# Kernel optimization log

Hardware: AMD Instinct MI355X
Metric: run time of the kernel (lower is better)

The kernel has to match this reference:

```python
import jax, jax.numpy as jnp
import numpy as np

B, C, S, L = 8, 512, 2048, 8921


def setup_inputs() -> dict:
    key = jax.random.key(0)
    k1, k2, k3, k4, k5 = jax.random.split(key, 5)
    return {
        "encoded": jax.random.normal(k1, (B, C, S), dtype=jnp.float32),
        "W_attn": jax.random.normal(k2, (L, C), dtype=jnp.float32) * 0.02,
        "b_attn": jax.random.normal(k3, (L,), dtype=jnp.float32) * 0.02,
        "W_cls": jax.random.normal(k4, (L, C), dtype=jnp.float32) * 0.02,
        "b_cls": jax.random.normal(k5, (L,), dtype=jnp.float32) * 0.02,
    }


def reference(encoded, W_attn, b_attn, W_cls, b_cls):
    # encoded: (B, C, S). Linear over channels after transpose -> scores (B, S, L)
    scores = jnp.einsum("bcs,lc->bsl", encoded, W_attn) + b_attn
    # softmax over the sequence dimension (dim=1 of (B, S, L))
    weights = jax.nn.softmax(scores, axis=1)
    # context: (B, L, S) @ (B, S, C) -> (B, L, C)
    context = jnp.einsum("bsl,bcs->blc", weights, encoded)
    # per-label diagonal classifier: elementwise multiply with (L, C) weight, reduce C
    logits = jnp.sum(context * W_cls, axis=2) + b_cls  # (B, L)
    return logits
```

## Files before the change

kernel.cpp:

```cpp
#include <hip/hip_runtime.h>
#include <hip/hip_bf16.h>
#include <stdint.h>

#define B_ 8
#define C_ 512
#define S_ 2048
#define L_ 8921
#define LTILE 128
#define NLT 70
#define BS 128
#define SCHUNK 512
#define NSC 4
#define STILES 4
#define BK 32
#define CITERS 16

using f32x4 = __attribute__((ext_vector_type(4))) float;
using s16x8 = __attribute__((ext_vector_type(8))) short;

static __device__ __forceinline__ unsigned short f2bf(float f) {
    union { float f; uint32_t u; } a; a.f = f;
    uint32_t u = a.u;
    return (unsigned short)((u + 0x7fffu + ((u >> 16) & 1u)) >> 16);
}

__global__ void cvt_w(const float* __restrict__ src, unsigned short* __restrict__ dst, int n4) {
    int i = blockIdx.x * 256 + threadIdx.x;
    if (i >= n4) return;
    float4 v = ((const float4*)src)[i];
    ushort4 o;
    o.x = f2bf(v.x); o.y = f2bf(v.y); o.z = f2bf(v.z); o.w = f2bf(v.w);
    ((ushort4*)dst)[i] = o;
}

__global__ void cvt_e(const float* __restrict__ enc, unsigned short* __restrict__ ebt) {
    __shared__ float tile[64][65];
    int x = blockIdx.x;
    int ct = (x & 7) * 64;
    int st = ((x >> 3) & 31) * 64;
    int b  = x >> 8;
    int t = threadIdx.x;
    const float* src = enc + (size_t)b * C_ * S_;
    #pragma unroll
    for (int it = 0; it < 16; ++it) {
        int idx = it * 256 + t;
        int rc = idx >> 6, rs = idx & 63;
        tile[rc][rs] = src[(size_t)(ct + rc) * S_ + st + rs];
    }
    __syncthreads();
    unsigned short* dst = ebt + (size_t)b * S_ * C_;
    #pragma unroll
    for (int it = 0; it < 16; ++it) {
        int idx = it * 256 + t;
        int rs = idx >> 6, rc = idx & 63;
        dst[(size_t)(st + rs) * C_ + ct + rc] = f2bf(tile[rc][rs]);
    }
}

__global__ __launch_bounds__(256, 2) void attn_main(
    const unsigned short* __restrict__ ebt,
    const unsigned short* __restrict__ wa,
    const unsigned short* __restrict__ wc,
    float* __restrict__ pnum, float* __restrict__ pden)
{
    __shared__ __align__(16) unsigned char smem[24576];
    unsigned char* sWa = smem;
    unsigned char* sWc = smem + 8192;
    unsigned char* sEt = smem + 16384;

    const int tid  = threadIdx.x;
    const int lane = tid & 63;
    const int wave = tid >> 6;

    const int x  = blockIdx.x;
    const int sc = x & 3;
    const int lt = (x >> 2) % NLT;
    const int b  = x / (NSC * NLT);

    const int l0 = lt * LTILE;
    const int wm = wave >> 1, wn = wave & 1;
    const int mbase = wm * 64, nbase = wn * 64;

    const int rowInSlab = lane >> 2;
    const int chunkGlb  = (lane & 3) ^ ((lane >> 3) & 3);
    const int fragKs  = (((lane >> 4) ^ ((lane >> 1) & 3)) << 4);
    const int fragRow = (lane & 15) << 6;

    float numAcc[4][4];
    float denAcc[4][4];
    #pragma unroll
    for (int i = 0; i < 4; ++i)
        #pragma unroll
        for (int r = 0; r < 4; ++r) { numAcc[i][r] = 0.f; denAcc[i][r] = 0.f; }

    for (int st = 0; st < STILES; ++st) {
        const int s0 = sc * SCHUNK + st * BS;
        f32x4 accS[4][4], accV[4][4];
        #pragma unroll
        for (int i = 0; i < 4; ++i)
            #pragma unroll
            for (int j = 0; j < 4; ++j) {
                accS[i][j] = (f32x4){0.f, 0.f, 0.f, 0.f};
                accV[i][j] = (f32x4){0.f, 0.f, 0.f, 0.f};
            }

        for (int ci = 0; ci < CITERS; ++ci) {
            const int c0 = ci * BK;
            __syncthreads();
            #pragma unroll
            for (int j = 0; j < 6; ++j) {
                const int slab = wave * 6 + j;
                const unsigned short* gsrc;
                unsigned char* ldst;
                if (slab < 8) {
                    int gl = l0 + slab * 16 + rowInSlab; if (gl > L_ - 1) gl = L_ - 1;
                    gsrc = wa + (size_t)gl * C_ + c0 + chunkGlb * 8;
                    ldst = sWa + slab * 1024;
                } else if (slab < 16) {
                    int g = slab - 8;
                    int gl = l0 + g * 16 + rowInSlab; if (gl > L_ - 1) gl = L_ - 1;
                    gsrc = wc + (size_t)gl * C_ + c0 + chunkGlb * 8;
                    ldst = sWc + g * 1024;
                } else {
                    int g = slab - 16;
                    int gs = s0 + g * 16 + rowInSlab;
                    gsrc = ebt + ((size_t)b * S_ + gs) * C_ + c0 + chunkGlb * 8;
                    ldst = sEt + g * 1024;
                }
                __builtin_amdgcn_global_load_lds(
                    (__attribute__((address_space(1))) void*)gsrc,
                    (__attribute__((address_space(3))) void*)ldst,
                    16, 0, 0);
            }
            __syncthreads();

            s16x8 fa[4], fc[4], fe[4];
            #pragma unroll
            for (int mf = 0; mf < 4; ++mf) {
                const int off = ((mbase + mf * 16) << 6) + fragRow + fragKs;
                fa[mf] = *(const s16x8*)(sWa + off);
                fc[mf] = *(const s16x8*)(sWc + off);
            }
            #pragma unroll
            for (int nf = 0; nf < 4; ++nf) {
                const int off = ((nbase + nf * 16) << 6) + fragRow + fragKs;
                fe[nf] = *(const s16x8*)(sEt + off);
            }
            #pragma unroll
            for (int mf = 0; mf < 4; ++mf)
                #pragma unroll
                for (int nf = 0; nf < 4; ++nf) {
                    accS[mf][nf] = __builtin_amdgcn_mfma_f32_16x16x32_bf16(fa[mf], fe[nf], accS[mf][nf], 0, 0, 0);
                    accV[mf][nf] = __builtin_amdgcn_mfma_f32_16x16x32_bf16(fc[mf], fe[nf], accV[mf][nf], 0, 0, 0);
                }
        }

        #pragma unroll
        for (int mf = 0; mf < 4; ++mf)
            #pragma unroll
            for (int nf = 0; nf < 4; ++nf)
                #pragma unroll
                for (int r = 0; r < 4; ++r) {
                    float e = __expf(accS[mf][nf][r]);
                    denAcc[mf][r] += e;
                    numAcc[mf][r] += e * accV[mf][nf][r];
                }
    }

    __syncthreads();
    float* pn = (float*)smem;
    float* pd = (float*)(smem + 1024);
    #pragma unroll
    for (int mf = 0; mf < 4; ++mf)
        #pragma unroll
        for (int r = 0; r < 4; ++r) {
            float n = numAcc[mf][r], d = denAcc[mf][r];
            n += __shfl_xor(n, 1);  d += __shfl_xor(d, 1);
            n += __shfl_xor(n, 2);  d += __shfl_xor(d, 2);
            n += __shfl_xor(n, 4);  d += __shfl_xor(d, 4);
            n += __shfl_xor(n, 8);  d += __shfl_xor(d, 8);
            if ((lane & 15) == 0) {
                int lrow = mf * 16 + (lane >> 4) * 4 + r;
                pn[wave * 64 + lrow] = n;
                pd[wave * 64 + lrow] = d;
            }
        }
    __syncthreads();
    if (tid < LTILE) {
        int half = tid >> 6;
        int lrow = tid & 63;
        float n = pn[(half * 2) * 64 + lrow] + pn[(half * 2 + 1) * 64 + lrow];
        float d = pd[(half * 2) * 64 + lrow] + pd[(half * 2 + 1) * 64 + lrow];
        size_t idx = ((size_t)((b * NLT + lt) * NSC + sc)) * LTILE + tid;
        pnum[idx] = n; pden[idx] = d;
    }
}

__global__ void finalize(const float* __restrict__ pnum, const float* __restrict__ pden,
                         const float* __restrict__ bcls, float* __restrict__ out) {
    int gid = blockIdx.x * 256 + threadIdx.x;
    if (gid >= B_ * L_) return;
    int b = gid / L_, l = gid - b * L_;
    int lt = l >> 7, row = l & 127;
    float n = 0.f, d = 0.f;
    #pragma unroll
    for (int s = 0; s < NSC; ++s) {
        size_t idx = ((size_t)((b * NLT + lt) * NSC + s)) * LTILE + row;
        n += pnum[idx];
        d += pden[idx];
    }
    out[gid] = n / d + bcls[l];
}

extern "C" void kernel_launch(void* const* d_in, const int* in_sizes, int n_in,
                              void* d_out, int out_size, void* d_ws, size_t ws_size,
                              hipStream_t stream) {
    (void)in_sizes; (void)n_in; (void)out_size; (void)ws_size;
    const float* enc  = (const float*)d_in[0];
    const float* Wa   = (const float*)d_in[1];
    const float* Wc   = (const float*)d_in[3];
    const float* bcls = (const float*)d_in[4];

    unsigned char* ws = (unsigned char*)d_ws;
    const size_t oEbt = 0;
    const size_t oWa  = oEbt + 16777216;
    const size_t oWc  = oWa + 9136128;
    const size_t oPn  = oWc + 9136128;
    const size_t oPd  = oPn + 1146880;

    unsigned short* ebt  = (unsigned short*)(ws + oEbt);
    unsigned short* waBf = (unsigned short*)(ws + oWa);
    unsigned short* wcBf = (unsigned short*)(ws + oWc);
    float* pnum = (float*)(ws + oPn);
    float* pden = (float*)(ws + oPd);

    const int n4 = (L_ * C_) / 4;
    cvt_w<<<(n4 + 255) / 256, 256, 0, stream>>>(Wa, waBf, n4);
    cvt_w<<<(n4 + 255) / 256, 256, 0, stream>>>(Wc, wcBf, n4);
    cvt_e<<<B_ * 32 * 8, 256, 0, stream>>>(enc, ebt);
    attn_main<<<B_ * NLT * NSC, 256, 0, stream>>>(ebt, waBf, wcBf, pnum, pden);
    finalize<<<(B_ * L_ + 255) / 256, 256, 0, stream>>>(pnum, pden, bcls, (float*)d_out);
}
```

Before: 478.3 us.

## Restructure attention GEMM: register-resident weight fragments, double-buffered LDS encoded tiles

Each wave now owns 32 label rows across the full 128-column s-tile. It loads its W_attn and W_cls fragments straight from global memory into registers and prefetches them one step ahead, so only the encoded tile is staged in LDS. That tile is double-buffered with a deeper K step of 64, which halves barriers and removes LDS traffic for the weights. Block order is remapped so that blocks sharing a label tile run together, for L2 reuse of the weights. In exchange the kernel carries more accumulator registers (16 accumulator tiles per wave) and relies on global loads to cover latency.

```diff
diff --git a/kernel.cpp b/kernel.cpp
--- a/kernel.cpp
+++ b/kernel.cpp
@@ -11,9 +11,8 @@
 #define BS 128
 #define SCHUNK 512
 #define NSC 4
-#define STILES 4
-#define BK 32
-#define CITERS 16
+#define BK 64
+#define ROUNDS 32
 
 using f32x4 = __attribute__((ext_vector_type(4))) float;
 using s16x8 = __attribute__((ext_vector_type(8))) short;
@@ -63,115 +62,135 @@
     const unsigned short* __restrict__ wc,
     float* __restrict__ pnum, float* __restrict__ pden)
 {
-    __shared__ __align__(16) unsigned char smem[24576];
-    unsigned char* sWa = smem;
-    unsigned char* sWc = smem + 8192;
-    unsigned char* sEt = smem + 16384;
+    __shared__ __align__(16) unsigned char sE[32768];
 
     const int tid  = threadIdx.x;
     const int lane = tid & 63;
     const int wave = tid >> 6;
 
     const int x  = blockIdx.x;
-    const int sc = x & 3;
-    const int lt = (x >> 2) % NLT;
-    const int b  = x / (NSC * NLT);
-
+    const int lt = x >> 5;
+    const int rb = x & 31;
+    const int b  = rb >> 2;
+    const int sc = rb & 3;
     const int l0 = lt * LTILE;
-    const int wm = wave >> 1, wn = wave & 1;
-    const int mbase = wm * 64, nbase = wn * 64;
-
-    const int rowInSlab = lane >> 2;
-    const int chunkGlb  = (lane & 3) ^ ((lane >> 3) & 3);
-    const int fragKs  = (((lane >> 4) ^ ((lane >> 1) & 3)) << 4);
-    const int fragRow = (lane & 15) << 6;
-
-    float numAcc[4][4];
-    float denAcc[4][4];
-    #pragma unroll
-    for (int i = 0; i < 4; ++i)
-        #pragma unroll
-        for (int r = 0; r < 4; ++r) { numAcc[i][r] = 0.f; denAcc[i][r] = 0.f; }
-
-    for (int st = 0; st < STILES; ++st) {
-        const int s0 = sc * SCHUNK + st * BS;
-        f32x4 accS[4][4], accV[4][4];
-        #pragma unroll
-        for (int i = 0; i < 4; ++i)
-            #pragma unroll
-            for (int j = 0; j < 4; ++j) {
-                accS[i][j] = (f32x4){0.f, 0.f, 0.f, 0.f};
-                accV[i][j] = (f32x4){0.f, 0.f, 0.f, 0.f};
-            }
-
-        for (int ci = 0; ci < CITERS; ++ci) {
-            const int c0 = ci * BK;
-            __syncthreads();
-            #pragma unroll
-            for (int j = 0; j < 6; ++j) {
-                const int slab = wave * 6 + j;
-                const unsigned short* gsrc;
-                unsigned char* ldst;
-                if (slab < 8) {
-                    int gl = l0 + slab * 16 + rowInSlab; if (gl > L_ - 1) gl = L_ - 1;
-                    gsrc = wa + (size_t)gl * C_ + c0 + chunkGlb * 8;
-                    ldst = sWa + slab * 1024;
-                } else if (slab < 16) {
-                    int g = slab - 8;
-                    int gl = l0 + g * 16 + rowInSlab; if (gl > L_ - 1) gl = L_ - 1;
-                    gsrc = wc + (size_t)gl * C_ + c0 + chunkGlb * 8;
-                    ldst = sWc + g * 1024;
-                } else {
-                    int g = slab - 16;
-                    int gs = s0 + g * 16 + rowInSlab;
-                    gsrc = ebt + ((size_t)b * S_ + gs) * C_ + c0 + chunkGlb * 8;
-                    ldst = sEt + g * 1024;
-                }
-                __builtin_amdgcn_global_load_lds(
-                    (__attribute__((address_space(1))) void*)gsrc,
-                    (__attribute__((address_space(3))) void*)ldst,
-                    16, 0, 0);
-            }
-            __syncthreads();
-
-            s16x8 fa[4], fc[4], fe[4];
-            #pragma unroll
-            for (int mf = 0; mf < 4; ++mf) {
-                const int off = ((mbase + mf * 16) << 6) + fragRow + fragKs;
-                fa[mf] = *(const s16x8*)(sWa + off);
-                fc[mf] = *(const s16x8*)(sWc + off);
-            }
-            #pragma unroll
-            for (int nf = 0; nf < 4; ++nf) {
-                const int off = ((nbase + nf * 16) << 6) + fragRow + fragKs;
-                fe[nf] = *(const s16x8*)(sEt + off);
-            }
-            #pragma unroll
-            for (int mf = 0; mf < 4; ++mf)
+
+    int rowOff[2];
+    #pragma unroll
+    for (int mf = 0; mf < 2; ++mf) {
+        int gl = l0 + wave * 32 + mf * 16 + (lane & 15);
+        if (gl > L_ - 1) gl = L_ - 1;
+        rowOff[mf] = gl * C_ + ((lane >> 4) << 3);
+    }
+
+    const size_t ebase = (size_t)b * S_ * C_;
+    const int kgsrcE = (((lane & 7) ^ ((lane >> 3) & 7)) << 3);
+    const int rowPart = (lane & 15) << 7;
+    const int laneQ = lane >> 4;
+    const int laneX = lane & 7;
+
+    struct W4 { s16x8 a0, a1, c0, c1; };
+    auto loadW = [&](int rr, int k) -> W4 {
+        const int co = ((rr & 7) << 6) + (k << 5);
+        W4 w;
+        w.a0 = *(const s16x8*)(wa + rowOff[0] + co);
+        w.a1 = *(const s16x8*)(wa + rowOff[1] + co);
+        w.c0 = *(const s16x8*)(wc + rowOff[0] + co);
+        w.c1 = *(const s16x8*)(wc + rowOff[1] + co);
+        return w;
+    };
+
+    auto stageE = [&](int rr2) {
+        const int c0s = (rr2 & 7) << 6;
+        const int sBase = sc * SCHUNK + (rr2 >> 3) * BS;
+        unsigned char* dbase = sE + ((rr2 & 1) << 14);
+        #pragma unroll
+        for (int jj = 0; jj < 4; ++jj) {
+            const int j = wave * 4 + jj;
+            const int sg = sBase + j * 8 + (lane >> 3);
+            const unsigned short* g = ebt + ebase + (size_t)sg * C_ + c0s + kgsrcE;
+            __builtin_amdgcn_global_load_lds(
+                (__attribute__((address_space(1))) void*)g,
+                (__attribute__((address_space(3))) void*)(dbase + j * 1024),
+                16, 0, 0);
+        }
+    };
+
+    f32x4 accS[2][8], accV[2][8];
+    #pragma unroll
+    for (int mf = 0; mf < 2; ++mf)
+        #pragma unroll
+        for (int nf = 0; nf < 8; ++nf) {
+            accS[mf][nf] = (f32x4){0.f, 0.f, 0.f, 0.f};
+            accV[mf][nf] = (f32x4){0.f, 0.f, 0.f, 0.f};
+        }
+    float numAcc[2][4], denAcc[2][4];
+    #pragma unroll
+    for (int mf = 0; mf < 2; ++mf)
+        #pragma unroll
+        for (int r = 0; r < 4; ++r) { numAcc[mf][r] = 0.f; denAcc[mf][r] = 0.f; }
+
+    stageE(0);
+    W4 wcur = loadW(0, 0);
+
+    for (int rr = 0; rr < ROUNDS; ++rr) {
+        __syncthreads();
+        if (rr + 1 < ROUNDS) stageE(rr + 1);
+        W4 wnxt = loadW(rr, 1);
+
+        const unsigned char* fb = sE + ((rr & 1) << 14);
+        {
+            s16x8 fe[8];
+            #pragma unroll
+            for (int nf = 0; nf < 8; ++nf) {
+                const int off = (nf << 11) + rowPart + ((((0 * 4) + laneQ) ^ laneX) << 4);
+                fe[nf] = *(const s16x8*)(fb + off);
+            }
+            #pragma unroll
+            for (int nf = 0; nf < 8; ++nf) {
+                accS[0][nf] = __builtin_amdgcn_mfma_f32_16x16x32_bf16(wcur.a0, fe[nf], accS[0][nf], 0, 0, 0);
+                accS[1][nf] = __builtin_amdgcn_mfma_f32_16x16x32_bf16(wcur.a1, fe[nf], accS[1][nf], 0, 0, 0);
+                accV[0][nf] = __builtin_amdgcn_mfma_f32_16x16x32_bf16(wcur.c0, fe[nf], accV[0][nf], 0, 0, 0);
+                accV[1][nf] = __builtin_amdgcn_mfma_f32_16x16x32_bf16(wcur.c1, fe[nf], accV[1][nf], 0, 0, 0);
+            }
+        }
+        W4 wfut = (rr + 1 < ROUNDS) ? loadW(rr + 1, 0) : wcur;
+        {
+            s16x8 fe[8];
+            #pragma unroll
+            for (int nf = 0; nf < 8; ++nf) {
+                const int off = (nf << 11) + rowPart + (((4 + laneQ) ^ laneX) << 4);
+                fe[nf] = *(const s16x8*)(fb + off);
+            }
+            #pragma unroll
+            for (int nf = 0; nf < 8; ++nf) {
+                accS[0][nf] = __builtin_amdgcn_mfma_f32_16x16x32_bf16(wnxt.a0, fe[nf], accS[0][nf], 0, 0, 0);
+                accS[1][nf] = __builtin_amdgcn_mfma_f32_16x16x32_bf16(wnxt.a1, fe[nf], accS[1][nf], 0, 0, 0);
+                accV[0][nf] = __builtin_amdgcn_mfma_f32_16x16x32_bf16(wnxt.c0, fe[nf], accV[0][nf], 0, 0, 0);
+                accV[1][nf] = __builtin_amdgcn_mfma_f32_16x16x32_bf16(wnxt.c1, fe[nf], accV[1][nf], 0, 0, 0);
+            }
+        }
+        wcur = wfut;
+
+        if ((rr & 7) == 7) {
+            #pragma unroll
+            for (int mf = 0; mf < 2; ++mf)
                 #pragma unroll
-                for (int nf = 0; nf < 4; ++nf) {
-                    accS[mf][nf] = __builtin_amdgcn_mfma_f32_16x16x32_bf16(fa[mf], fe[nf], accS[mf][nf], 0, 0, 0);
-                    accV[mf][nf] = __builtin_amdgcn_mfma_f32_16x16x32_bf16(fc[mf], fe[nf], accV[mf][nf], 0, 0, 0);
-                }
-        }
-
-        #pragma unroll
-        for (int mf = 0; mf < 4; ++mf)
-            #pragma unroll
-            for (int nf = 0; nf < 4; ++nf)
-                #pragma unroll
-                for (int r = 0; r < 4; ++r) {
-                    float e = __expf(accS[mf][nf][r]);
-                    denAcc[mf][r] += e;
-                    numAcc[mf][r] += e * accV[mf][nf][r];
-                }
-    }
-
-    __syncthreads();
-    float* pn = (float*)smem;
-    float* pd = (float*)(smem + 1024);
-    #pragma unroll
-    for (int mf = 0; mf < 4; ++mf)
+                for (int nf = 0; nf < 8; ++nf)
+                    #pragma unroll
+                    for (int r = 0; r < 4; ++r) {
+                        float e = __expf(accS[mf][nf][r]);
+                        denAcc[mf][r] += e;
+                        numAcc[mf][r] += e * accV[mf][nf][r];
+                        accS[mf][nf][r] = 0.f;
+                        accV[mf][nf][r] = 0.f;
+                    }
+        }
+    }
+
+    const size_t obase = ((size_t)((b * NLT + lt) * NSC + sc)) * LTILE;
+    #pragma unroll
+    for (int mf = 0; mf < 2; ++mf)
         #pragma unroll
         for (int r = 0; r < 4; ++r) {
             float n = numAcc[mf][r], d = denAcc[mf][r];
@@ -180,20 +199,11 @@
             n += __shfl_xor(n, 4);  d += __shfl_xor(d, 4);
             n += __shfl_xor(n, 8);  d += __shfl_xor(d, 8);
             if ((lane & 15) == 0) {
-                int lrow = mf * 16 + (lane >> 4) * 4 + r;
-                pn[wave * 64 + lrow] = n;
-                pd[wave * 64 + lrow] = d;
-            }
-        }
-    __syncthreads();
-    if (tid < LTILE) {
-        int half = tid >> 6;
-        int lrow = tid & 63;
-        float n = pn[(half * 2) * 64 + lrow] + pn[(half * 2 + 1) * 64 + lrow];
-        float d = pd[(half * 2) * 64 + lrow] + pd[(half * 2 + 1) * 64 + lrow];
-        size_t idx = ((size_t)((b * NLT + lt) * NSC + sc)) * LTILE + tid;
-        pnum[idx] = n; pden[idx] = d;
-    }
+                int row = wave * 32 + mf * 16 + (lane >> 4) * 4 + r;
+                pnum[obase + row] = n;
+                pden[obase + row] = d;
+            }
+        }
 }
 
 __global__ void finalize(const float* __restrict__ pnum, const float* __restrict__ pden,
@@ -238,6 +248,6 @@
     cvt_w<<<(n4 + 255) / 256, 256, 0, stream>>>(Wa, waBf, n4);
     cvt_w<<<(n4 + 255) / 256, 256, 0, stream>>>(Wc, wcBf, n4);
     cvt_e<<<B_ * 32 * 8, 256, 0, stream>>>(enc, ebt);
-    attn_main<<<B_ * NLT * NSC, 256, 0, stream>>>(ebt, waBf, wcBf, pnum, pden);
+    attn_main<<<NLT * 32, 256, 0, stream>>>(ebt, waBf, wcBf, pnum, pden);
     finalize<<<(B_ * L_ + 255) / 256, 256, 0, stream>>>(pnum, pden, bcls, (float*)d_out);
 }
```

Result: faster. 433.5 us (-9.4%).

## Double-buffer LDS staging, switch to 32x32 MFMA, split S into 16 chunks

Applied to the files above, without the earlier changes.

The main kernel now double-buffers the LDS tiles so the global-to-LDS load for the next C slice overlaps with the MFMA work on the current one, removing one barrier per iteration. It switches from 16x16x32 to 32x32x16 bf16 MFMA to cut fragment loads per FLOP. Each block now handles a single 128-wide S tile, and the grid is reordered so blocks sharing an L tile run close together for weight reuse in L2. The cost is four times more partial sums for finalize, doubled LDS (48KB) that may limit occupancy, and more blocks that each re-stage the weight tiles.

```diff
diff --git a/kernel.cpp b/kernel.cpp
--- a/kernel.cpp
+++ b/kernel.cpp
@@ -8,15 +8,12 @@
 #define L_ 8921
 #define LTILE 128
 #define NLT 70
-#define BS 128
-#define SCHUNK 512
-#define NSC 4
-#define STILES 4
-#define BK 32
-#define CITERS 16
-
-using f32x4 = __attribute__((ext_vector_type(4))) float;
-using s16x8 = __attribute__((ext_vector_type(8))) short;
+#define NSC 16
+#define ROUNDS 16
+
+using f32x4  = __attribute__((ext_vector_type(4))) float;
+using f32x16 = __attribute__((ext_vector_type(16))) float;
+using s16x8  = __attribute__((ext_vector_type(8))) short;
 
 static __device__ __forceinline__ unsigned short f2bf(float f) {
     union { float f; uint32_t u; } a; a.f = f;
@@ -63,134 +60,136 @@
     const unsigned short* __restrict__ wc,
     float* __restrict__ pnum, float* __restrict__ pden)
 {
-    __shared__ __align__(16) unsigned char smem[24576];
-    unsigned char* sWa = smem;
-    unsigned char* sWc = smem + 8192;
-    unsigned char* sEt = smem + 16384;
+    __shared__ __align__(16) unsigned char smem[49152];
 
     const int tid  = threadIdx.x;
     const int lane = tid & 63;
     const int wave = tid >> 6;
 
     const int x  = blockIdx.x;
-    const int sc = x & 3;
-    const int lt = (x >> 2) % NLT;
-    const int b  = x / (NSC * NLT);
-
+    const int lt = x >> 7;
+    const int b  = (x >> 4) & 7;
+    const int sc = x & 15;
     const int l0 = lt * LTILE;
+    const int s0 = sc * 128;
     const int wm = wave >> 1, wn = wave & 1;
-    const int mbase = wm * 64, nbase = wn * 64;
-
-    const int rowInSlab = lane >> 2;
-    const int chunkGlb  = (lane & 3) ^ ((lane >> 3) & 3);
-    const int fragKs  = (((lane >> 4) ^ ((lane >> 1) & 3)) << 4);
-    const int fragRow = (lane & 15) << 6;
-
-    float numAcc[4][4];
-    float denAcc[4][4];
-    #pragma unroll
-    for (int i = 0; i < 4; ++i)
-        #pragma unroll
-        for (int r = 0; r < 4; ++r) { numAcc[i][r] = 0.f; denAcc[i][r] = 0.f; }
-
-    for (int st = 0; st < STILES; ++st) {
-        const int s0 = sc * SCHUNK + st * BS;
-        f32x4 accS[4][4], accV[4][4];
-        #pragma unroll
-        for (int i = 0; i < 4; ++i)
+
+    const int slRow = lane >> 2;
+    const int srcCk = ((lane & 3) ^ (slRow & 3)) * 8;
+
+    const unsigned short* slabG[6];
+    int slabL[6];
+    #pragma unroll
+    for (int j = 0; j < 6; ++j) {
+        const int slab = wave * 6 + j;
+        if (slab < 8) {
+            int gl = l0 + slab * 16 + slRow; if (gl > L_ - 1) gl = L_ - 1;
+            slabG[j] = wa + (size_t)gl * C_ + srcCk;
+            slabL[j] = slab * 1024;
+        } else if (slab < 16) {
+            int g = slab - 8;
+            int gl = l0 + g * 16 + slRow; if (gl > L_ - 1) gl = L_ - 1;
+            slabG[j] = wc + (size_t)gl * C_ + srcCk;
+            slabL[j] = 8192 + g * 1024;
+        } else {
+            int g = slab - 16;
+            int gs = s0 + g * 16 + slRow;
+            slabG[j] = ebt + ((size_t)b * S_ + gs) * C_ + srcCk;
+            slabL[j] = 16384 + g * 1024;
+        }
+    }
+
+    auto stage = [&](int rr) {
+        const int c0 = rr * 32;
+        const int bufo = (rr & 1) * 24576;
+        #pragma unroll
+        for (int j = 0; j < 6; ++j) {
+            __builtin_amdgcn_global_load_lds(
+                (__attribute__((address_space(1))) void*)(slabG[j] + c0),
+                (__attribute__((address_space(3))) void*)(smem + bufo + slabL[j]),
+                16, 0, 0);
+        }
+    };
+
+    const int p0   = (lane & 31) * 64;
+    const int xorc = lane & 3;
+    const int h    = lane >> 5;
+    const int aOff0 = (wm * 64) * 64;
+    const int aOff1 = (wm * 64 + 32) * 64;
+    const int eOff0 = (wn * 64) * 64;
+    const int eOff1 = (wn * 64 + 32) * 64;
+
+    f32x16 accS[2][2], accV[2][2];
+    #pragma unroll
+    for (int mt = 0; mt < 2; ++mt)
+        #pragma unroll
+        for (int nt = 0; nt < 2; ++nt)
             #pragma unroll
-            for (int j = 0; j < 4; ++j) {
-                accS[i][j] = (f32x4){0.f, 0.f, 0.f, 0.f};
-                accV[i][j] = (f32x4){0.f, 0.f, 0.f, 0.f};
-            }
-
-        for (int ci = 0; ci < CITERS; ++ci) {
-            const int c0 = ci * BK;
-            __syncthreads();
-            #pragma unroll
-            for (int j = 0; j < 6; ++j) {
-                const int slab = wave * 6 + j;
-                const unsigned short* gsrc;
-                unsigned char* ldst;
-                if (slab < 8) {
-                    int gl = l0 + slab * 16 + rowInSlab; if (gl > L_ - 1) gl = L_ - 1;
-                    gsrc = wa + (size_t)gl * C_ + c0 + chunkGlb * 8;
-                    ldst = sWa + slab * 1024;
-                } else if (slab < 16) {
-                    int g = slab - 8;
-                    int gl = l0 + g * 16 + rowInSlab; if (gl > L_ - 1) gl = L_ - 1;
-                    gsrc = wc + (size_t)gl * C_ + c0 + chunkGlb * 8;
-                    ldst = sWc + g * 1024;
-                } else {
-                    int g = slab - 16;
-                    int gs = s0 + g * 16 + rowInSlab;
-                    gsrc = ebt + ((size_t)b * S_ + gs) * C_ + c0 + chunkGlb * 8;
-                    ldst = sEt + g * 1024;
-                }
-                __builtin_amdgcn_global_load_lds(
-                    (__attribute__((address_space(1))) void*)gsrc,
-                    (__attribute__((address_space(3))) void*)ldst,
-                    16, 0, 0);
-            }
-            __syncthreads();
-
-            s16x8 fa[4], fc[4], fe[4];
-            #pragma unroll
-            for (int mf = 0; mf < 4; ++mf) {
-                const int off = ((mbase + mf * 16) << 6) + fragRow + fragKs;
-                fa[mf] = *(const s16x8*)(sWa + off);
-                fc[mf] = *(const s16x8*)(sWc + off);
-            }
-            #pragma unroll
-            for (int nf = 0; nf < 4; ++nf) {
-                const int off = ((nbase + nf * 16) << 6) + fragRow + fragKs;
-                fe[nf] = *(const s16x8*)(sEt + off);
-            }
-            #pragma unroll
-            for (int mf = 0; mf < 4; ++mf)
-                #pragma unroll
-                for (int nf = 0; nf < 4; ++nf) {
-                    accS[mf][nf] = __builtin_amdgcn_mfma_f32_16x16x32_bf16(fa[mf], fe[nf], accS[mf][nf], 0, 0, 0);
-                    accV[mf][nf] = __builtin_amdgcn_mfma_f32_16x16x32_bf16(fc[mf], fe[nf], accV[mf][nf], 0, 0, 0);
-                }
-        }
-
-        #pragma unroll
-        for (int mf = 0; mf < 4; ++mf)
-            #pragma unroll
-            for (int nf = 0; nf < 4; ++nf)
-                #pragma unroll
-                for (int r = 0; r < 4; ++r) {
-                    float e = __expf(accS[mf][nf][r]);
-                    denAcc[mf][r] += e;
-                    numAcc[mf][r] += e * accV[mf][nf][r];
-                }
-    }
-
+            for (int r = 0; r < 16; ++r) { accS[mt][nt][r] = 0.f; accV[mt][nt][r] = 0.f; }
+
+    stage(0);
     __syncthreads();
+
+    for (int rr = 0; rr < ROUNDS; ++rr) {
+        if (rr + 1 < ROUNDS) stage(rr + 1);
+        const unsigned char* db = smem + (rr & 1) * 24576;
+        const unsigned char* dWa = db;
+        const unsigned char* dWc = db + 8192;
+        const unsigned char* dE  = db + 16384;
+        #pragma unroll
+        for (int j = 0; j < 2; ++j) {
+            const int ck = (((2 * j) + h) ^ xorc) * 16;
+            s16x8 fa0 = *(const s16x8*)(dWa + aOff0 + p0 + ck);
+            s16x8 fa1 = *(const s16x8*)(dWa + aOff1 + p0 + ck);
+            s16x8 fc0 = *(const s16x8*)(dWc + aOff0 + p0 + ck);
+            s16x8 fc1 = *(const s16x8*)(dWc + aOff1 + p0 + ck);
+            s16x8 fe0 = *(const s16x8*)(dE  + eOff0 + p0 + ck);
+            s16x8 fe1 = *(const s16x8*)(dE  + eOff1 + p0 + ck);
+            accS[0][0] = __builtin_amdgcn_mfma_f32_32x32x16_bf16(fa0, fe0, accS[0][0], 0, 0, 0);
+            accS[0][1] = __builtin_amdgcn_mfma_f32_32x32x16_bf16(fa0, fe1, accS[0][1], 0, 0, 0);
+            accS[1][0] = __builtin_amdgcn_mfma_f32_32x32x16_bf16(fa1, fe0, accS[1][0], 0, 0, 0);
+            accS[1][1] = __builtin_amdgcn_mfma_f32_32x32x16_bf16(fa1, fe1, accS[1][1], 0, 0, 0);
+            accV[0][0] = __builtin_amdgcn_mfma_f32_32x32x16_bf16(fc0, fe0, accV[0][0], 0, 0, 0);
+            accV[0][1] = __builtin_amdgcn_mfma_f32_32x32x16_bf16(fc0, fe1, accV[0][1], 0, 0, 0);
+            accV[1][0] = __builtin_amdgcn_mfma_f32_32x32x16_bf16(fc1, fe0, accV[1][0], 0, 0, 0);
+            accV[1][1] = __builtin_amdgcn_mfma_f32_32x32x16_bf16(fc1, fe1, accV[1][1], 0, 0, 0);
+        }
+        __syncthreads();
+    }
+
+    float rn[2][16], rd[2][16];
+    #pragma unroll
+    for (int mt = 0; mt < 2; ++mt)
+        #pragma unroll
+        for (int r = 0; r < 16; ++r) {
+            float e0 = __expf(accS[mt][0][r]);
+            float e1 = __expf(accS[mt][1][r]);
+            float n = e0 * accV[mt][0][r] + e1 * accV[mt][1][r];
+            float d = e0 + e1;
+            n += __shfl_xor(n, 1);   d += __shfl_xor(d, 1);
+            n += __shfl_xor(n, 2);   d += __shfl_xor(d, 2);
+            n += __shfl_xor(n, 4);   d += __shfl_xor(d, 4);
+            n += __shfl_xor(n, 8);   d += __shfl_xor(d, 8);
+            n += __shfl_xor(n, 16);  d += __shfl_xor(d, 16);
+            rn[mt][r] = n; rd[mt][r] = d;
+        }
+
     float* pn = (float*)smem;
     float* pd = (float*)(smem + 1024);
-    #pragma unroll
-    for (int mf = 0; mf < 4; ++mf)
-        #pragma unroll
-        for (int r = 0; r < 4; ++r) {
-            float n = numAcc[mf][r], d = denAcc[mf][r];
-            n += __shfl_xor(n, 1);  d += __shfl_xor(d, 1);
-            n += __shfl_xor(n, 2);  d += __shfl_xor(d, 2);
-            n += __shfl_xor(n, 4);  d += __shfl_xor(d, 4);
-            n += __shfl_xor(n, 8);  d += __shfl_xor(d, 8);
-            if ((lane & 15) == 0) {
-                int lrow = mf * 16 + (lane >> 4) * 4 + r;
-                pn[wave * 64 + lrow] = n;
-                pd[wave * 64 + lrow] = d;
+    if ((lane & 31) == 0) {
+        #pragma unroll
+        for (int mt = 0; mt < 2; ++mt)
+            #pragma unroll
+            for (int r = 0; r < 16; ++r) {
+                int row = wm * 64 + mt * 32 + (r & 3) + 8 * (r >> 2) + 4 * h;
+                pn[wn * 128 + row] = rn[mt][r];
+                pd[wn * 128 + row] = rd[mt][r];
             }
-        }
+    }
     __syncthreads();
     if (tid < LTILE) {
-        int half = tid >> 6;
-        int lrow = tid & 63;
-        float n = pn[(half * 2) * 64 + lrow] + pn[(half * 2 + 1) * 64 + lrow];
-        float d = pd[(half * 2) * 64 + lrow] + pd[(half * 2 + 1) * 64 + lrow];
+        float n = pn[tid] + pn[128 + tid];
+        float d = pd[tid] + pd[128 + tid];
         size_t idx = ((size_t)((b * NLT + lt) * NSC + sc)) * LTILE + tid;
         pnum[idx] = n; pden[idx] = d;
     }
@@ -226,7 +225,7 @@
     const size_t oWa  = oEbt + 16777216;
     const size_t oWc  = oWa + 9136128;
     const size_t oPn  = oWc + 9136128;
-    const size_t oPd  = oPn + 1146880;
+    const size_t oPd  = oPn + 4587520;
 
     unsigned short* ebt  = (unsigned short*)(ws + oEbt);
     unsigned short* waBf = (unsigned short*)(ws + oWa);
@@ -238,6 +237,6 @@
     cvt_w<<<(n4 + 255) / 256, 256, 0, stream>>>(Wa, waBf, n4);
     cvt_w<<<(n4 + 255) / 256, 256, 0, stream>>>(Wc, wcBf, n4);
     cvt_e<<<B_ * 32 * 8, 256, 0, stream>>>(enc, ebt);
-    attn_main<<<B_ * NLT * NSC, 256, 0, stream>>>(ebt, waBf, wcBf, pnum, pden);
+    attn_main<<<NLT * 128, 256, 0, stream>>>(ebt, waBf, wcBf, pnum, pden);
     finalize<<<(B_ * L_ + 255) / 256, 256, 0, stream>>>(pnum, pden, bcls, (float*)d_out);
 }
```

After: 528.0 us. +10.4%, slower.
